# Kernel tuning notes

Measured on AMD Instinct MI355X. Metric: run time of the kernel, lower is better.

Reference implementation:

```python
import jax, jax.numpy as jnp
import numpy as np

EPS = 1e-15
PROJ_EPS = 4e-3  # float32 eps used by PoincareBall.proj

def artanh(x):
    x = jnp.clip(x, -1.0 + EPS, 1.0 - EPS)
    return 0.5 * (jnp.log1p(x) - jnp.log1p(-x))

def poincare_proj(x, c):
    # clip points to stay strictly inside the ball of radius 1/sqrt(c)
    norm = jnp.maximum(jnp.linalg.norm(x, axis=-1, keepdims=True), EPS)
    maxnorm = (1.0 - PROJ_EPS) / jnp.sqrt(c)
    return jnp.where(norm > maxnorm, x / norm * maxnorm, x)

def mobius_add(x, y, c):
    # x, y broadcast to [..., dim]
    x2 = jnp.sum(x * x, axis=-1, keepdims=True)
    y2 = jnp.sum(y * y, axis=-1, keepdims=True)
    xy = jnp.sum(x * y, axis=-1, keepdims=True)
    num = (1.0 + 2.0 * c * xy + c * y2) * x + (1.0 - c * x2) * y
    denom = 1.0 + 2.0 * c * xy + (c ** 2) * x2 * y2
    return num / jnp.maximum(denom, EPS)

def poincare_sqdist(x, y, c):
    sqrt_c = jnp.sqrt(c)
    diff_norm = jnp.linalg.norm(mobius_add(-x, y, c), axis=-1)
    dist = 2.0 / sqrt_c * artanh(sqrt_c * diff_norm)
    return dist ** 2

def setup_inputs() -> dict:
    key = jax.random.key(0)
    k1, k2 = jax.random.split(key)
    N, K, D = 8192, 256, 128
    node_repr = jax.random.normal(k1, (N, D), dtype=jnp.float32) * 0.01  # points near origin of the ball
    centroid_weight = jax.random.normal(k2, (K, D), dtype=jnp.float32) * 0.01
    mask = jnp.ones((N, 1), dtype=jnp.float32)
    c = jnp.ones((1,), dtype=jnp.float32)
    return {"node_repr": node_repr, "mask": mask, "centroid_weight": centroid_weight, "c": c}

def reference(node_repr, mask, centroid_weight, c):
    cc = c[0]
    centroid_repr = poincare_proj(centroid_weight, cc)            # [K, D]
    # broadcasted pairwise hyperbolic squared distances: [N, K]
    node_centroid_dist = poincare_sqdist(node_repr[:, None, :], centroid_repr[None, :, :], cc)
    node_centroid_dist = node_centroid_dist[None]                  # [1, N, K]
    graph_centroid_dist = jnp.sum(node_centroid_dist, axis=1) / jnp.sum(mask)  # [1, K]
    return (graph_centroid_dist, node_centroid_dist)
```

## Files before the change

kernel.cpp:

```cpp
#include <hip/hip_runtime.h>
#include <hip/hip_bf16.h>
#include <math.h>

#define KTOT 256
#define TN 64
#define TK 64

typedef __attribute__((ext_vector_type(8))) short bf16x8;
typedef __attribute__((ext_vector_type(4))) float f32x4;

static __device__ __forceinline__ bf16x8 pack8(float4 a, float4 b) {
    union { __hip_bfloat162 h[4]; bf16x8 v; } u;
    u.h[0] = __float22bfloat162_rn(make_float2(a.x, a.y));
    u.h[1] = __float22bfloat162_rn(make_float2(a.z, a.w));
    u.h[2] = __float22bfloat162_rn(make_float2(b.x, b.y));
    u.h[3] = __float22bfloat162_rn(make_float2(b.z, b.w));
    return u.v;
}
static __device__ __forceinline__ float sq4(float4 v) {
    return fmaf(v.x, v.x, fmaf(v.y, v.y, fmaf(v.z, v.z, v.w * v.w)));
}

__global__ __launch_bounds__(256) void scd_fused(
    const float* __restrict__ node,
    const float* __restrict__ maskp,
    const float* __restrict__ cw,
    const float* __restrict__ cptr,
    float* __restrict__ out,
    unsigned* __restrict__ cnt,
    float* __restrict__ part,
    int nbn, int nblk, int maskN)
{
    __shared__ short xs[TN][128];
    __shared__ short ys[TK][128];
    __shared__ float x2_s[TN];
    __shared__ float y2r_s[TK];
    __shared__ float part_s[4][TK];
    __shared__ float wred[4];
    __shared__ int lastblk;

    const int tid = threadIdx.x;
    const int w = tid >> 6, l = tid & 63;
    const int q = l >> 4, r15 = l & 15;
    const int bn = blockIdx.x >> 2, kq = blockIdx.x & 3;
    const int nb = bn * TN, kb = kq * TK;
    const float c = cptr[0];

    float mp = 0.f;
    {
        const float4* m4 = (const float4*)maskp;
        int m4n = maskN >> 2;
        for (int e = tid; e < m4n; e += 256) {
            float4 v = m4[e];
            mp += (v.x + v.y) + (v.z + v.w);
        }
    }

    const float4* nf4 = (const float4*)(node + (size_t)nb * 128);
    #pragma unroll
    for (int i = 0; i < 4; ++i) {
        int e = tid + 256 * i;
        int r = e >> 4, j = e & 15;
        float4 a = nf4[r * 32 + j * 2];
        float4 b = nf4[r * 32 + j * 2 + 1];
        float p = sq4(a) + sq4(b);
        p += __shfl_xor(p, 1);
        p += __shfl_xor(p, 2);
        p += __shfl_xor(p, 4);
        p += __shfl_xor(p, 8);
        if ((tid & 15) == 0) x2_s[r] = p;
        *(bf16x8*)&xs[r][8 * (j ^ (r & 15))] = pack8(a, b);
    }
    const float4* yf4 = (const float4*)(cw + (size_t)kb * 128);
    #pragma unroll
    for (int i = 0; i < 4; ++i) {
        int e = tid + 256 * i;
        int r = e >> 4, j = e & 15;
        float4 a = yf4[r * 32 + j * 2];
        float4 b = yf4[r * 32 + j * 2 + 1];
        float p = sq4(a) + sq4(b);
        p += __shfl_xor(p, 1);
        p += __shfl_xor(p, 2);
        p += __shfl_xor(p, 4);
        p += __shfl_xor(p, 8);
        if ((tid & 15) == 0) y2r_s[r] = p;
        *(bf16x8*)&ys[r][8 * (j ^ (r & 15))] = pack8(a, b);
    }
    __syncthreads();

    const int rA = 16 * w + r15;
    const int key = r15;

    f32x4 acc[4];
    #pragma unroll
    for (int ct = 0; ct < 4; ++ct) acc[ct] = (f32x4){0.f, 0.f, 0.f, 0.f};

    #pragma unroll
    for (int ks = 0; ks < 4; ++ks) {
        int jl = q + 4 * ks;
        bf16x8 A = *(bf16x8*)&xs[rA][8 * (jl ^ key)];
        #pragma unroll
        for (int ct = 0; ct < 4; ++ct) {
            bf16x8 B = *(bf16x8*)&ys[16 * ct + r15][8 * (jl ^ key)];
            acc[ct] = __builtin_amdgcn_mfma_f32_16x16x32_bf16(A, B, acc[ct], 0, 0, 0);
        }
    }

    const float sqrt_c = sqrtf(c);
    const float maxn = (1.0f - 4e-3f) / sqrt_c;
    const float dscale = (2.0f * 0.34657359028f) / sqrt_c;
    const float twoc = 2.0f * c;
    const float cc2 = c * c;

    float scv[4], y2v[4], abase[4], ccy2[4];
    #pragma unroll
    for (int ct = 0; ct < 4; ++ct) {
        float ss = y2r_s[16 * ct + r15];
        float nrm = fmaxf(sqrtf(ss), 1e-15f);
        float sc = (nrm > maxn) ? maxn * __builtin_amdgcn_rcpf(nrm) : 1.0f;
        scv[ct] = sc;
        y2v[ct] = ss * sc * sc;
        abase[ct] = fmaf(c, y2v[ct], 1.0f);
        ccy2[ct] = cc2 * y2v[ct];
    }

    float kpart[4] = {0.f, 0.f, 0.f, 0.f};
    #pragma unroll
    for (int reg = 0; reg < 4; ++reg) {
        const int rl = 4 * q + reg;
        const float x2 = x2_s[16 * w + rl];
        const float b = fmaf(-c, x2, 1.0f);
        float* po = out + KTOT + (size_t)(nb + 16 * w + rl) * KTOT + kb + r15;
        #pragma unroll
        for (int ct = 0; ct < 4; ++ct) {
            float xy = -acc[ct][reg] * scv[ct];
            float a = fmaf(twoc, xy, abase[ct]);
            float den = fmaf(twoc, xy, fmaf(ccy2[ct], x2, 1.0f));
            float num2 = fmaf(a * a, x2, fmaf(b * b, y2v[ct], 2.0f * a * b * xy));
            num2 = fmaxf(num2, 0.0f);
            den = fmaxf(den, 1e-15f);
            float z = sqrt_c * __builtin_amdgcn_sqrtf(num2) * __builtin_amdgcn_rcpf(den);
            z = fminf(fmaxf(z, 0.0f), 0.99999994f);
            float arg = (1.0f + z) * __builtin_amdgcn_rcpf(1.0f - z);
            float d = dscale * __builtin_amdgcn_logf(arg);
            float s = d * d;
            po[16 * ct] = s;
            kpart[ct] += s;
        }
    }

    #pragma unroll
    for (int ct = 0; ct < 4; ++ct) {
        kpart[ct] += __shfl_xor(kpart[ct], 16);
        kpart[ct] += __shfl_xor(kpart[ct], 32);
    }
    mp += __shfl_xor(mp, 1);  mp += __shfl_xor(mp, 2);  mp += __shfl_xor(mp, 4);
    mp += __shfl_xor(mp, 8);  mp += __shfl_xor(mp, 16); mp += __shfl_xor(mp, 32);
    if (l == 0) wred[w] = mp;
    if (l < 16) {
        #pragma unroll
        for (int ct = 0; ct < 4; ++ct) part_s[w][16 * ct + l] = kpart[ct];
    }
    __syncthreads();
    if (tid < TK) {
        float v = (part_s[0][tid] + part_s[1][tid]) + (part_s[2][tid] + part_s[3][tid]);
        __hip_atomic_store(&part[(size_t)bn * KTOT + kb + tid], v,
                           __ATOMIC_RELAXED, __HIP_MEMORY_SCOPE_AGENT);
    }

    __syncthreads();
    if (tid == 0) {
        unsigned old = __hip_atomic_fetch_add(cnt, 1u, __ATOMIC_RELAXED, __HIP_MEMORY_SCOPE_AGENT);
        lastblk = ((old % (unsigned)nblk) == (unsigned)(nblk - 1));
    }
    __syncthreads();
    if (!lastblk) return;

    float msum = (wred[0] + wred[1]) + (wred[2] + wred[3]);
    float inv = 1.0f / msum;

    const float* pc = part + tid;
    float s[16];
    #pragma unroll
    for (int u = 0; u < 16; ++u)
        s[u] = __hip_atomic_load(pc + (size_t)u * KTOT, __ATOMIC_RELAXED, __HIP_MEMORY_SCOPE_AGENT);
    for (int g = 16; g < nbn; g += 16)
        #pragma unroll
        for (int u = 0; u < 16; ++u)
            s[u] += __hip_atomic_load(pc + (size_t)(g + u) * KTOT, __ATOMIC_RELAXED, __HIP_MEMORY_SCOPE_AGENT);
    float t0 = ((s[0] + s[1]) + (s[2] + s[3])) + ((s[4] + s[5]) + (s[6] + s[7]));
    float t1 = ((s[8] + s[9]) + (s[10] + s[11])) + ((s[12] + s[13]) + (s[14] + s[15]));
    out[tid] = (t0 + t1) * inv;
}

extern "C" void kernel_launch(void* const* d_in, const int* in_sizes, int n_in,
                              void* d_out, int out_size, void* d_ws, size_t ws_size,
                              hipStream_t stream) {
    const float* node = (const float*)d_in[0];
    const float* mask = (const float*)d_in[1];
    const float* cw   = (const float*)d_in[2];
    const float* cp   = (const float*)d_in[3];
    float* out = (float*)d_out;
    unsigned* cnt = (unsigned*)d_ws;
    float* part = (float*)((char*)d_ws + 256);

    int N = in_sizes[0] / 128;
    int maskN = in_sizes[1];
    int nbn = N / TN;
    int nblk = nbn * (KTOT / TK);

    scd_fused<<<dim3(nblk), 256, 0, stream>>>(node, mask, cw, cp, out, cnt, part,
                                              nbn, nblk, maskN);
}
```

Before: 19.21 us.

## Remap centroid columns so each lane stores a float4 of contiguous outputs

Reorders the centroid tile so that lane r15 handles centroids 4*r15..4*r15+3 across the four MFMA column tiles. Each lane can then write its four distances as one float4 store instead of four strided scalar stores, and the LDS swizzle for the centroid tile is adjusted to match. It also folds the artanh ratio into (den+t)/(den-t), which drops one reciprocal and the clamp, and widens the final partial-sum reduction in the last block to 32 independent loads. The risk is LDS bank conflicts from the new row mapping and slightly different numerics near the ball boundary.

```diff
diff --git a/kernel.cpp b/kernel.cpp
--- a/kernel.cpp
+++ b/kernel.cpp
@@ -84,12 +84,11 @@
         p += __shfl_xor(p, 4);
         p += __shfl_xor(p, 8);
         if ((tid & 15) == 0) y2r_s[r] = p;
-        *(bf16x8*)&ys[r][8 * (j ^ (r & 15))] = pack8(a, b);
+        *(bf16x8*)&ys[r][8 * (j ^ ((r >> 2) & 15))] = pack8(a, b);
     }
     __syncthreads();
 
     const int rA = 16 * w + r15;
-    const int key = r15;
 
     f32x4 acc[4];
     #pragma unroll
@@ -98,10 +97,10 @@
     #pragma unroll
     for (int ks = 0; ks < 4; ++ks) {
         int jl = q + 4 * ks;
-        bf16x8 A = *(bf16x8*)&xs[rA][8 * (jl ^ key)];
+        bf16x8 A = *(bf16x8*)&xs[rA][8 * (jl ^ r15)];
         #pragma unroll
         for (int ct = 0; ct < 4; ++ct) {
-            bf16x8 B = *(bf16x8*)&ys[16 * ct + r15][8 * (jl ^ key)];
+            bf16x8 B = *(bf16x8*)&ys[4 * r15 + ct][8 * (jl ^ r15)];
             acc[ct] = __builtin_amdgcn_mfma_f32_16x16x32_bf16(A, B, acc[ct], 0, 0, 0);
         }
     }
@@ -115,7 +114,7 @@
     float scv[4], y2v[4], abase[4], ccy2[4];
     #pragma unroll
     for (int ct = 0; ct < 4; ++ct) {
-        float ss = y2r_s[16 * ct + r15];
+        float ss = y2r_s[4 * r15 + ct];
         float nrm = fmaxf(sqrtf(ss), 1e-15f);
         float sc = (nrm > maxn) ? maxn * __builtin_amdgcn_rcpf(nrm) : 1.0f;
         scv[ct] = sc;
@@ -130,23 +129,25 @@
         const int rl = 4 * q + reg;
         const float x2 = x2_s[16 * w + rl];
         const float b = fmaf(-c, x2, 1.0f);
-        float* po = out + KTOT + (size_t)(nb + 16 * w + rl) * KTOT + kb + r15;
+        const float bb = b * b;
+        float sv[4];
         #pragma unroll
         for (int ct = 0; ct < 4; ++ct) {
             float xy = -acc[ct][reg] * scv[ct];
             float a = fmaf(twoc, xy, abase[ct]);
             float den = fmaf(twoc, xy, fmaf(ccy2[ct], x2, 1.0f));
-            float num2 = fmaf(a * a, x2, fmaf(b * b, y2v[ct], 2.0f * a * b * xy));
+            float num2 = fmaf(a * a, x2, fmaf(bb, y2v[ct], 2.0f * a * b * xy));
             num2 = fmaxf(num2, 0.0f);
             den = fmaxf(den, 1e-15f);
-            float z = sqrt_c * __builtin_amdgcn_sqrtf(num2) * __builtin_amdgcn_rcpf(den);
-            z = fminf(fmaxf(z, 0.0f), 0.99999994f);
-            float arg = (1.0f + z) * __builtin_amdgcn_rcpf(1.0f - z);
+            float t = sqrt_c * __builtin_amdgcn_sqrtf(num2);
+            float arg = (den + t) * __builtin_amdgcn_rcpf(fmaxf(den - t, 1e-30f));
             float d = dscale * __builtin_amdgcn_logf(arg);
             float s = d * d;
-            po[16 * ct] = s;
+            sv[ct] = s;
             kpart[ct] += s;
         }
+        *(float4*)(out + KTOT + (size_t)(nb + 16 * w + rl) * KTOT + kb + 4 * r15)
+            = make_float4(sv[0], sv[1], sv[2], sv[3]);
     }
 
     #pragma unroll
@@ -159,7 +160,7 @@
     if (l == 0) wred[w] = mp;
     if (l < 16) {
         #pragma unroll
-        for (int ct = 0; ct < 4; ++ct) part_s[w][16 * ct + l] = kpart[ct];
+        for (int ct = 0; ct < 4; ++ct) part_s[w][4 * l + ct] = kpart[ct];
     }
     __syncthreads();
     if (tid < TK) {
@@ -180,17 +181,22 @@
     float inv = 1.0f / msum;
 
     const float* pc = part + tid;
-    float s[16];
-    #pragma unroll
-    for (int u = 0; u < 16; ++u)
+    float s[32];
+    #pragma unroll
+    for (int u = 0; u < 32; ++u)
         s[u] = __hip_atomic_load(pc + (size_t)u * KTOT, __ATOMIC_RELAXED, __HIP_MEMORY_SCOPE_AGENT);
-    for (int g = 16; g < nbn; g += 16)
-        #pragma unroll
-        for (int u = 0; u < 16; ++u)
+    int g = 32;
+    for (; g + 31 < nbn; g += 32)
+        #pragma unroll
+        for (int u = 0; u < 32; ++u)
             s[u] += __hip_atomic_load(pc + (size_t)(g + u) * KTOT, __ATOMIC_RELAXED, __HIP_MEMORY_SCOPE_AGENT);
-    float t0 = ((s[0] + s[1]) + (s[2] + s[3])) + ((s[4] + s[5]) + (s[6] + s[7]));
-    float t1 = ((s[8] + s[9]) + (s[10] + s[11])) + ((s[12] + s[13]) + (s[14] + s[15]));
-    out[tid] = (t0 + t1) * inv;
+    for (; g < nbn; ++g)
+        s[0] += __hip_atomic_load(pc + (size_t)g * KTOT, __ATOMIC_RELAXED, __HIP_MEMORY_SCOPE_AGENT);
+    #pragma unroll
+    for (int st = 16; st > 0; st >>= 1)
+        #pragma unroll
+        for (int u = 0; u < st; ++u) s[u] += s[u + st];
+    out[tid] = s[0] * inv;
 }
 
 extern "C" void kernel_launch(void* const* d_in, const int* in_sizes, int n_in,
```

After: 17.96 us. -6.5%, faster.
